# Optimization experiments

Measured on AMD Instinct MI355X. Metric: run time of the kernel, lower is better.

The kernel has to match this reference:

```python
import jax, jax.numpy as jnp
import numpy as np

N, E, B = 50000, 800000, 128
NF, ED, HID, HEADS, DH, OUT, L = 7, 2, 128, 4, 32, 64, 3
EPS = 1e-5
NEG_SLOPE = 0.2


def _layer_norm(x, g, b):
    mu = jnp.mean(x, axis=-1, keepdims=True)
    v = jnp.mean((x - mu) ** 2, axis=-1, keepdims=True)
    return g * (x - mu) / jnp.sqrt(v + EPS) + b


def setup_inputs() -> dict:
    key = jax.random.key(0)
    ks = jax.random.split(key, 32)
    s = 0.05
    inp = {
        "x": jax.random.normal(ks[0], (N, NF), jnp.float32),
        "edge_index": jax.random.randint(ks[1], (2, E), 0, N, jnp.int32),
        "edge_attr": jax.random.uniform(ks[2], (E, ED), jnp.float32),
        "batch": jnp.sort(jax.random.randint(ks[3], (N,), 0, B, jnp.int32)),
        # node encoder
        "enc_W": jax.random.normal(ks[4], (NF, HID)) * (1.0 / np.sqrt(NF)),
        "enc_b": jnp.zeros((HID,)),
        "enc_g": jnp.ones((HID,)),
        "enc_bb": jnp.zeros((HID,)),
        # GATv2 layers (stacked over L)
        "gat_Wsrc": jax.random.normal(ks[5], (L, HID, HID)) * (1.0 / np.sqrt(HID)),
        "gat_Wdst": jax.random.normal(ks[6], (L, HID, HID)) * (1.0 / np.sqrt(HID)),
        "gat_We": jax.random.normal(ks[7], (L, ED, HID)) * (1.0 / np.sqrt(ED)),
        "gat_att": jax.random.normal(ks[8], (L, HEADS, DH)) * s,
        "gat_bias": jnp.zeros((L, HID)),
        # GraphNorm per layer
        "gn_w": jnp.ones((L, HID)),
        "gn_b": jnp.zeros((L, HID)),
        "gn_s": jnp.ones((L, HID)),  # mean_scale
        # attention pooling
        "pool_W1": jax.random.normal(ks[9], (HID, HID)) * (1.0 / np.sqrt(HID)),
        "pool_b1": jnp.zeros((HID,)),
        "pool_W2": jax.random.normal(ks[10], (HID, 1)) * (1.0 / np.sqrt(HID)),
        # output mapper
        "map_W1": jax.random.normal(ks[11], (HID, HID)) * (1.0 / np.sqrt(HID)),
        "map_b1": jnp.zeros((HID,)),
        "map_g": jnp.ones((HID,)),
        "map_bb": jnp.zeros((HID,)),
        "map_W2": jax.random.normal(ks[12], (HID, OUT)) * (1.0 / np.sqrt(HID)),
        "map_b2": jnp.zeros((OUT,)),
    }
    return inp


def _segment_softmax(scores, seg, num_seg):
    # scores: [E2, HEADS], seg: [E2] destination node ids
    m = jax.ops.segment_max(scores, seg, num_segments=num_seg)
    ex = jnp.exp(scores - m[seg])
    denom = jax.ops.segment_sum(ex, seg, num_segments=num_seg)
    return ex / denom[seg]


def _gatv2(x, src, dst, ea, Wsrc, Wdst, We, att, bias):
    e2 = src.shape[0]
    xl = (x @ Wsrc)[src].reshape(e2, HEADS, DH)   # lin_l(x_j), source
    xr = (x @ Wdst)[dst].reshape(e2, HEADS, DH)   # lin_r(x_i), target
    ee = (ea @ We).reshape(e2, HEADS, DH)
    z = jax.nn.leaky_relu(xl + xr + ee, NEG_SLOPE)
    score = jnp.einsum("ehd,hd->eh", z, att)
    alpha = _segment_softmax(score, dst, N)       # softmax over incoming edges
    msg = (xl * alpha[:, :, None]).reshape(e2, HID)
    out = jax.ops.segment_sum(msg, dst, num_segments=N)
    return out + bias


def _graph_norm(x, batch, w, b, scale):
    cnt = jax.ops.segment_sum(jnp.ones((N,), x.dtype), batch, num_segments=B)
    cnt = jnp.maximum(cnt, 1.0)[:, None]
    mean = jax.ops.segment_sum(x, batch, num_segments=B) / cnt
    xc = x - scale * mean[batch]
    var = jax.ops.segment_sum(xc * xc, batch, num_segments=B) / cnt
    return w * xc / jnp.sqrt(var[batch] + EPS) + b


def reference(x, edge_index, edge_attr, batch, enc_W, enc_b, enc_g, enc_bb,
              gat_Wsrc, gat_Wdst, gat_We, gat_att, gat_bias, gn_w, gn_b, gn_s,
              pool_W1, pool_b1, pool_W2, map_W1, map_b1, map_g, map_bb,
              map_W2, map_b2):
    # node encoder: Linear -> ReLU -> LayerNorm
    h = _layer_norm(jax.nn.relu(x @ enc_W + enc_b), enc_g, enc_bb)

    # add self loops; self-loop edge_attr = mean of edge_attr (PyG fill_value='mean')
    loop = jnp.arange(N, dtype=edge_index.dtype)
    src = jnp.concatenate([edge_index[0], loop])
    dst = jnp.concatenate([edge_index[1], loop])
    ea_mean = jnp.mean(edge_attr, axis=0)
    ea = jnp.concatenate([edge_attr, jnp.broadcast_to(ea_mean, (N, ED))], axis=0)

    for i in range(L):
        out = _gatv2(h, src, dst, ea, gat_Wsrc[i], gat_Wdst[i], gat_We[i],
                     gat_att[i], gat_bias[i])
        out = out + h  # residual (in_dim == out_dim -> Identity proj)
        out = _graph_norm(out, batch, gn_w[i], gn_b[i], gn_s[i])
        h = jax.nn.elu(out)

    node_emb = h
    # attention pooling: softmax over ALL nodes (dim=0, as in source)
    scores = jnp.tanh(h @ pool_W1 + pool_b1) @ pool_W2          # [N, 1]
    weights = jax.nn.softmax(scores, axis=0)
    g = jax.ops.segment_sum(h * weights, batch, num_segments=B)  # [B, HID]

    # output mapper (dropout inactive at eval)
    g = _layer_norm(jax.nn.relu(g @ map_W1 + map_b1), map_g, map_bb)
    graph_emb = g @ map_W2 + map_b2
    return graph_emb, node_emb
```

## Files before the change

### kernel.cpp

```cpp
#include <hip/hip_runtime.h>
#include <hip/hip_bf16.h>

typedef __hip_bfloat16 bf16;
typedef __attribute__((ext_vector_type(8))) short short8;
typedef __attribute__((ext_vector_type(4))) float float4v;
typedef float f32x2 __attribute__((ext_vector_type(2)));

#define Nn   50000
#define Ee   800000
#define E2   850000
#define Bb   128
#define NFd  7
#define HID  128
#define OUTD 64
#define EPS  1e-5f
#define SLOPE 0.2f
#define LOG2E 1.4426950408889634f
#define NSTRIP 3125
#define NPAIR  1563

#define MFMA16(a,b,c) __builtin_amdgcn_mfma_f32_16x16x32_bf16(a,b,c,0,0,0)

__device__ __forceinline__ float lane_bcast(float v, int l){
  return __int_as_float(__builtin_amdgcn_readlane(__float_as_int(v), l));
}
__device__ __forceinline__ float wred_sum(float v){
  #pragma unroll
  for (int o=32;o;o>>=1) v += __shfl_xor(v, o, 64);
  return v;
}
#define UPD_DPP(x, ctrl) \
  __int_as_float(__builtin_amdgcn_update_dpp(0, __float_as_int(x), (ctrl), 0xf, 0xf, false))
__device__ __forceinline__ float red4_quad(float x){
  x = x + UPD_DPP(x, 0xB1);
  x = x + UPD_DPP(x, 0x4E);
  return x;
}
__device__ __forceinline__ unsigned fkey(float f){
  unsigned u = __float_as_uint(f);
  return (u & 0x80000000u) ? ~u : (u | 0x80000000u);
}
__device__ __forceinline__ float fkeyinv(unsigned k){
  unsigned u = (k & 0x80000000u) ? (k ^ 0x80000000u) : ~k;
  return __uint_as_float(u);
}
__device__ __forceinline__ float tanh_fast(float x){
  float e = __expf(fminf(fmaxf(2.f*x, -30.f), 30.f));
  return (e-1.f)/(e+1.f);
}
__device__ __forceinline__ float bf_lo(unsigned u){ return __uint_as_float(u<<16); }
__device__ __forceinline__ float bf_hi(unsigned u){ return __uint_as_float(u & 0xffff0000u); }
__device__ __forceinline__ unsigned short f2bs(float f){
  bf16 h = __float2bfloat16(f);
  return *reinterpret_cast<unsigned short*>(&h);
}
__device__ __forceinline__ unsigned pack2(float a, float b){
  return (unsigned)f2bs(a) | ((unsigned)f2bs(b) << 16);
}
__device__ __forceinline__ int xcd_swizzle(int bid, int nwg){
  int q = nwg >> 3, r = nwg & 7;
  int x = bid & 7, i = bid >> 3;
  return (x < r ? x*(q+1) : r*(q+1) + (x-r)*q) + i;
}

__global__ __launch_bounds__(256) void k_wprep(
    const float* __restrict__ gWsrc, const float* __restrict__ gWdst,
    const float* __restrict__ pW1,
    unsigned* __restrict__ wtimg, unsigned* __restrict__ pw1img){
  int idx = blockIdx.x*256 + threadIdx.x;
  if (idx < 3*256*64){
    int l  = idx / (256*64);
    int r  = idx - l*(256*64);
    int n  = r >> 6;
    int kp = r & 63;
    const float* Wp = (n < 128) ? (gWsrc + (size_t)l*HID*HID)
                                : (gWdst + (size_t)l*HID*HID - 128);
    float w0 = Wp[(2*kp)*HID + n];
    float w1 = Wp[(2*kp+1)*HID + n];
    int byt = (n*256 + kp*4) ^ ((n&7)<<4);
    *(unsigned*)((char*)(wtimg + (size_t)l*16384) + byt) = pack2(w0, w1);
  } else {
    int r = idx - 3*256*64;
    if (r < 128*64){
      int n  = r >> 6;
      int kp = r & 63;
      float w0 = pW1[(2*kp)*HID + n];
      float w1 = pW1[(2*kp+1)*HID + n];
      int byt = (n*256 + kp*4) ^ ((n&7)<<4);
      *(unsigned*)((char*)pw1img + byt) = pack2(w0, w1);
    }
  }
}

__global__ __launch_bounds__(256) void k_encoder(
    const float* __restrict__ x, const float* __restrict__ W, const float* __restrict__ b,
    const float* __restrict__ g, const float* __restrict__ bbv,
    unsigned* __restrict__ hbu){
  int wv = (blockIdx.x*blockDim.x + threadIdx.x) >> 6;
  if (wv >= Nn) return;
  int lane = threadIdx.x & 63;
  int d0 = 2*lane, d1 = d0+1;
  float y0 = b[d0], y1 = b[d1];
  #pragma unroll
  for (int i=0;i<NFd;++i){
    float xv = x[wv*NFd + i];
    y0 = fmaf(xv, W[i*HID + d0], y0);
    y1 = fmaf(xv, W[i*HID + d1], y1);
  }
  y0 = fmaxf(y0, 0.f); y1 = fmaxf(y1, 0.f);
  float mu = wred_sum(y0+y1) * (1.f/HID);
  float c0 = y0-mu, c1 = y1-mu;
  float var = wred_sum(c0*c0 + c1*c1) * (1.f/HID);
  float rs = rsqrtf(var + EPS);
  float v0 = g[d0]*c0*rs + bbv[d0];
  float v1 = g[d1]*c1*rs + bbv[d1];
  hbu[(size_t)wv*64 + lane] = pack2(v0, v1);
}

__global__ void k_ea_mean(const float* __restrict__ ea, float* __restrict__ eam){
  int tid = blockIdx.x*blockDim.x + threadIdx.x;
  const float2* ea2 = (const float2*)ea;
  float a0=0.f, a1=0.f;
  for (int e=tid; e<Ee; e += gridDim.x*blockDim.x){
    float2 v = ea2[e];
    a0 += v.x; a1 += v.y;
  }
  a0 = wred_sum(a0); a1 = wred_sum(a1);
  if ((threadIdx.x & 63)==0){
    atomicAdd(&eam[0], a0*(1.f/Ee));
    atomicAdd(&eam[1], a1*(1.f/Ee));
  }
}

__global__ void k_deg(const int* __restrict__ ei, int* __restrict__ deg){
  int e = blockIdx.x*blockDim.x + threadIdx.x;
  if (e >= E2) return;
  int d = (e < Ee) ? ei[Ee + e] : (e - Ee);
  atomicAdd(&deg[d], 1);
}

__global__ __launch_bounds__(1024) void k_scan(const int* __restrict__ deg,
    int* __restrict__ offs, int* __restrict__ cursor){
  __shared__ int wsum[16];
  __shared__ int tot_s;
  __shared__ int carry_s;
  int t = threadIdx.x, lane = t & 63, wid = t >> 6;
  if (t==0) carry_s = 0;
  __syncthreads();
  for (int base=0; base<Nn; base += 4096){
    int i0 = base + t*4;
    int v0=0,v1=0,v2=0,v3=0;
    if (i0+3 < Nn){
      int4 qv = *(const int4*)(deg + i0);
      v0=qv.x; v1=qv.y; v2=qv.z; v3=qv.w;
    } else {
      if (i0   < Nn) v0 = deg[i0];
      if (i0+1 < Nn) v1 = deg[i0+1];
      if (i0+2 < Nn) v2 = deg[i0+2];
      if (i0+3 < Nn) v3 = deg[i0+3];
    }
    int tot = v0+v1+v2+v3;
    int x = tot;
    #pragma unroll
    for (int o=1;o<64;o<<=1){ int u = __shfl_up(x, o, 64); if (lane >= o) x += u; }
    if (lane==63) wsum[wid] = x;
    __syncthreads();
    if (t==0){ int s=0; for (int k=0;k<16;++k){ int tv=wsum[k]; wsum[k]=s; s+=tv; } tot_s = s; }
    __syncthreads();
    int excl = carry_s + wsum[wid] + (x - tot);
    int p0 = excl, p1 = excl+v0, p2 = p1+v1, p3 = p2+v2;
    if (i0+3 < Nn){
      *(int4*)(offs + i0)   = make_int4(p0,p1,p2,p3);
      *(int4*)(cursor + i0) = make_int4(p0,p1,p2,p3);
    } else {
      if (i0   < Nn){ offs[i0]  =p0; cursor[i0]  =p0; }
      if (i0+1 < Nn){ offs[i0+1]=p1; cursor[i0+1]=p1; }
      if (i0+2 < Nn){ offs[i0+2]=p2; cursor[i0+2]=p2; }
      if (i0+3 < Nn){ offs[i0+3]=p3; cursor[i0+3]=p3; }
    }
    __syncthreads();
    if (t==0) carry_s += tot_s;
    __syncthreads();
  }
  if (t==0) offs[Nn] = carry_s;
}

__global__ void k_scatter(const int* __restrict__ ei, const float* __restrict__ ea,
    const float* __restrict__ eam, int* __restrict__ cursor,
    int* __restrict__ csrc, float2* __restrict__ cea){
  int e = blockIdx.x*blockDim.x + threadIdx.x;
  if (e >= E2 + 8) return;
  if (e >= E2){
    csrc[e] = 0;
    cea[e] = make_float2(0.f, 0.f);
    return;
  }
  int s, d; float a0, a1;
  if (e < Ee){
    s = ei[e]; d = ei[Ee + e];
    float2 v = ((const float2*)ea)[e];
    a0 = v.x; a1 = v.y;
  } else {
    s = d = e - Ee; a0 = eam[0]; a1 = eam[1];
  }
  int pos = atomicAdd(&cursor[d], 1);
  csrc[pos] = s;
  cea[pos] = make_float2(a0, a1);
}

__global__ void k_gstart(const int* __restrict__ batch, int* __restrict__ gstart){
  int n = blockIdx.x*blockDim.x + threadIdx.x;
  if (n >= Nn) return;
  int bc = batch[n];
  int bp = (n==0) ? -1 : batch[n-1];
  for (int b = bp+1; b <= bc; ++b) gstart[b] = n;
  if (n == Nn-1){ for (int b = bc+1; b <= Bb; ++b) gstart[b] = Nn; }
}

__global__ __launch_bounds__(256) void k_dualgemm(
    const unsigned* __restrict__ hbu, const unsigned* __restrict__ wtimg,
    unsigned* __restrict__ hsb, float* __restrict__ hd){
  __shared__ unsigned wt[16384];
  for (int i = threadIdx.x; i < 4096; i += 256)
    ((uint4*)wt)[i] = ((const uint4*)wtimg)[i];
  __syncthreads();
  int wid = threadIdx.x >> 6, lane = threadIdx.x & 63;
  int q = lane >> 4, c = lane & 15;
  const unsigned short* hb = (const unsigned short*)hbu;
  for (int pr = blockIdx.x*4 + wid; pr < NPAIR; pr += gridDim.x*4){
    int p0 = 2*pr, p1 = 2*pr + 1;
    bool v1 = (p1 < NSTRIP);
    int node0 = p0*16 + c;
    int node1 = v1 ? (p1*16 + c) : node0;
    short8 bf0[4], bf1[4];
    const unsigned short* hp0 = hb + (size_t)node0*HID + q*8;
    const unsigned short* hp1 = hb + (size_t)node1*HID + q*8;
    #pragma unroll
    for (int s=0;s<4;++s){
      bf0[s] = *(const short8*)(hp0 + s*32);
      bf1[s] = *(const short8*)(hp1 + s*32);
    }
    #pragma unroll 4
    for (int t=0;t<16;++t){
      float4v ac0 = {0.f,0.f,0.f,0.f}, ac1 = {0.f,0.f,0.f,0.f};
      #pragma unroll
      for (int s=0;s<4;++s){
        int row = t*16 + c;
        int byt = (row*256 + s*64 + q*16) ^ ((row&7)<<4);
        short8 af = *(const short8*)((const char*)wt + byt);
        ac0 = MFMA16(af, bf0[s], ac0);
        ac1 = MFMA16(af, bf1[s], ac1);
      }
      if (t < 8){
        int co = t*8 + q*2;
        *(uint2*)(hsb + (size_t)node0*64 + co) =
            make_uint2(pack2(ac0[0],ac0[1]), pack2(ac0[2],ac0[3]));
        if (v1) *(uint2*)(hsb + (size_t)node1*64 + co) =
            make_uint2(pack2(ac1[0],ac1[1]), pack2(ac1[2],ac1[3]));
      } else {
        int dd = (t-8)*16 + q*4;
        *(float4*)(hd + (size_t)node0*HID + dd) = make_float4(ac0[0],ac0[1],ac0[2],ac0[3]);
        if (v1) *(float4*)(hd + (size_t)node1*HID + dd) = make_float4(ac1[0],ac1[1],ac1[2],ac1[3]);
      }
    }
  }
}

__global__ __launch_bounds__(256) void k_edge(const unsigned* __restrict__ hsb,
    float* __restrict__ hdio, const unsigned* __restrict__ hbu,
    const int* __restrict__ csrc, const float2* __restrict__ cea,
    const int* __restrict__ offs, const float* __restrict__ We,
    const float* __restrict__ att, const float* __restrict__ bias){
  int bid = xcd_swizzle(blockIdx.x, gridDim.x);
  int n = (bid*256 + (int)threadIdx.x) >> 6;
  if (n >= Nn) return;
  int lane = threadIdx.x & 63;
  int row = lane >> 4;
  int c   = lane & 15;
  int d0  = 8*c;
  f32x2 we0v[4], we1v[4], atv[4], xrv[4];
  #pragma unroll
  for (int k=0;k<4;++k){
    we0v[k] = *(const f32x2*)(We + d0 + 2*k);
    we1v[k] = *(const f32x2*)(We + HID + d0 + 2*k);
    f32x2 a = *(const f32x2*)(att + d0 + 2*k);
    atv[k]  = a * LOG2E;
    xrv[k]  = *(const f32x2*)(hdio + (size_t)n*HID + d0 + 2*k);
  }
  int e0 = offs[n], e1 = offs[n+1];
  float m = 0.f, ssum = 0.f;
  f32x2 accv[4];
  #pragma unroll
  for (int k=0;k<4;++k) accv[k] = (f32x2){0.f,0.f};

  int   sC = csrc[e0 + row];
  float2 eC = cea[e0 + row];
  uint4 xC = *(const uint4*)(hsb + ((size_t)(unsigned)sC<<6) + 4*c);
  bool  vC = (e0 + row) < e1;
  for (int e = e0; e < e1; e += 4){
    int en = e + 4 + row;
    int   sN = csrc[en];
    float2 eN = cea[en];
    uint4 xN = *(const uint4*)(hsb + ((size_t)(unsigned)sN<<6) + 4*c);
    bool  vN = en < e1;
    f32x2 xl2[4];
    xl2[0] = (f32x2){bf_lo(xC.x), bf_hi(xC.x)};
    xl2[1] = (f32x2){bf_lo(xC.y), bf_hi(xC.y)};
    xl2[2] = (f32x2){bf_lo(xC.z), bf_hi(xC.z)};
    xl2[3] = (f32x2){bf_lo(xC.w), bf_hi(xC.w)};
    f32x2 ex2 = (f32x2){eC.x, eC.x};
    f32x2 ey2 = (f32x2){eC.y, eC.y};
    f32x2 dotv = (f32x2){0.f, 0.f};
    #pragma unroll
    for (int k=0;k<4;++k){
      f32x2 z = __builtin_elementwise_fma(ey2, we1v[k],
                  __builtin_elementwise_fma(ex2, we0v[k], xl2[k] + xrv[k]));
      z = __builtin_elementwise_max(z, z * SLOPE);
      dotv = __builtin_elementwise_fma(z, atv[k], dotv);
    }
    float sc = red4_quad(dotv.x + dotv.y);
    if (e == e0) m = __shfl(sc, lane & 15, 64);
    float p = exp2f(sc - m);
    p = vC ? p : 0.f;
    ssum += p;
    f32x2 pv = (f32x2){p, p};
    #pragma unroll
    for (int k=0;k<4;++k) accv[k] = __builtin_elementwise_fma(pv, xl2[k], accv[k]);
    sC=sN; eC=eN; xC=xN; vC=vN;
  }
  float acc[8];
  #pragma unroll
  for (int k=0;k<4;++k){ acc[2*k] = accv[k].x; acc[2*k+1] = accv[k].y; }
  #pragma unroll
  for (int j=0;j<8;++j){
    acc[j] += __shfl_xor(acc[j], 16, 64);
    acc[j] += __shfl_xor(acc[j], 32, 64);
  }
  ssum += __shfl_xor(ssum, 16, 64);
  ssum += __shfl_xor(ssum, 32, 64);
  if (row == 0){
    float inv = 1.f/ssum;
    uint4 hu = *(const uint4*)(hbu + ((size_t)n<<6) + 4*c);
    float hr[8];
    hr[0]=bf_lo(hu.x); hr[1]=bf_hi(hu.x); hr[2]=bf_lo(hu.y); hr[3]=bf_hi(hu.y);
    hr[4]=bf_lo(hu.z); hr[5]=bf_hi(hu.z); hr[6]=bf_lo(hu.w); hr[7]=bf_hi(hu.w);
    float o[8];
    #pragma unroll
    for (int j=0;j<8;++j) o[j] = fmaf(acc[j], inv, bias[d0+j] + hr[j]);
    *(float4*)(hdio + (size_t)n*HID + d0)     = make_float4(o[0],o[1],o[2],o[3]);
    *(float4*)(hdio + (size_t)n*HID + d0 + 4) = make_float4(o[4],o[5],o[6],o[7]);
  }
}

__global__ __launch_bounds__(128) void k_gn_reduce(const float* __restrict__ out,
    const int* __restrict__ gstart, float* __restrict__ gsum_, float* __restrict__ gsq_){
  int b = blockIdx.x >> 4, sub = blockIdx.x & 15;
  int ns = gstart[b], ne = gstart[b+1];
  int d = threadIdx.x;
  float s = 0.f, qq = 0.f;
  for (int n = ns + sub; n < ne; n += 16){
    float v = out[(size_t)n*HID + d];
    s += v; qq = fmaf(v, v, qq);
  }
  atomicAdd(&gsum_[b*HID + d], s);
  atomicAdd(&gsq_[b*HID + d], qq);
}

__global__ __launch_bounds__(256) void k_gn_apply(const float* __restrict__ out,
    const float* __restrict__ gsum_, const float* __restrict__ gsq_,
    const int* __restrict__ gstart, const int* __restrict__ batch,
    const float* __restrict__ gw, const float* __restrict__ gb,
    const float* __restrict__ gs,
    unsigned* __restrict__ hbu, float* __restrict__ emb){
  int n = (blockIdx.x*blockDim.x + threadIdx.x) >> 6;
  if (n >= Nn) return;
  int lane = threadIdx.x & 63;
  int b = batch[n];
  float icnt = 1.f / fmaxf((float)(gstart[b+1]-gstart[b]), 1.f);
  int d0 = 2*lane, d1 = d0+1;
  float2 x = *(const float2*)(out + (size_t)n*HID + d0);
  float mean0 = gsum_[b*HID+d0]*icnt, mean1 = gsum_[b*HID+d1]*icnt;
  float ms0 = mean0*gs[d0], ms1 = mean1*gs[d1];
  float var0 = gsq_[b*HID+d0]*icnt - ms0*(2.f*mean0 - ms0);
  float var1 = gsq_[b*HID+d1]*icnt - ms1*(2.f*mean1 - ms1);
  float rs0 = rsqrtf(fmaxf(var0, 0.f) + EPS);
  float rs1 = rsqrtf(fmaxf(var1, 0.f) + EPS);
  float y0 = gw[d0]*(x.x - ms0)*rs0 + gb[d0];
  float y1 = gw[d1]*(x.y - ms1)*rs1 + gb[d1];
  y0 = (y0 > 0.f) ? y0 : (__expf(y0) - 1.f);
  y1 = (y1 > 0.f) ? y1 : (__expf(y1) - 1.f);
  hbu[(size_t)n*64 + lane] = pack2(y0, y1);
  if (emb) *(float2*)(emb + (size_t)n*HID + d0) = make_float2(y0, y1);
}

__global__ __launch_bounds__(256) void k_pool_score(
    const unsigned* __restrict__ hbu, const unsigned* __restrict__ pw1img,
    const float* __restrict__ b1, const float* __restrict__ W2,
    float* __restrict__ score, unsigned* __restrict__ mkey){
  __shared__ unsigned wt[8192];
  __shared__ float b1l[HID], w2l[HID];
  for (int i = threadIdx.x; i < 2048; i += 256)
    ((uint4*)wt)[i] = ((const uint4*)pw1img)[i];
  if (threadIdx.x < HID){ b1l[threadIdx.x] = b1[threadIdx.x]; w2l[threadIdx.x] = W2[threadIdx.x]; }
  __syncthreads();
  int wid = threadIdx.x >> 6, lane = threadIdx.x & 63;
  int q = lane >> 4, c = lane & 15;
  const unsigned short* hb = (const unsigned short*)hbu;
  float bmax = -1e30f;
  for (int p = blockIdx.x*4 + wid; p < NSTRIP; p += gridDim.x*4){
    int node = p*16 + c;
    short8 bf[4];
    const unsigned short* hp = hb + (size_t)node*HID + q*8;
    #pragma unroll
    for (int s=0;s<4;++s) bf[s] = *(const short8*)(hp + s*32);
    float part = 0.f;
    #pragma unroll
    for (int t=0;t<8;++t){
      float4v ac = {0.f,0.f,0.f,0.f};
      #pragma unroll
      for (int s=0;s<4;++s){
        int row = t*16 + c;
        int byt = (row*256 + s*64 + q*16) ^ ((row&7)<<4);
        ac = MFMA16(*(const short8*)((const char*)wt + byt), bf[s], ac);
      }
      int dim = t*16 + q*4;
      #pragma unroll
      for (int r=0;r<4;++r)
        part += tanh_fast(ac[r] + b1l[dim+r]) * w2l[dim+r];
    }
    part += __shfl_xor(part, 16, 64);
    part += __shfl_xor(part, 32, 64);
    if (q==0) score[node] = part;
    bmax = fmaxf(bmax, part);
  }
  #pragma unroll
  for (int o=32;o;o>>=1) bmax = fmaxf(bmax, __shfl_xor(bmax, o, 64));
  if (lane==0) atomicMax(mkey, fkey(bmax));
}

__global__ __launch_bounds__(128) void k_pool_reduce(const unsigned* __restrict__ hbu,
    const float* __restrict__ score, const unsigned* __restrict__ mkey,
    const int* __restrict__ gstart, float* __restrict__ gsum, float* __restrict__ total){
  int b = blockIdx.x >> 4, sub = blockIdx.x & 15;
  int ns = gstart[b], ne = gstart[b+1];
  float mx = fkeyinv(*mkey);
  int d = threadIdx.x;
  float acc = 0.f, es = 0.f;
  for (int n = ns + sub; n < ne; n += 16){
    float ev = __expf(score[n] - mx);
    unsigned u = hbu[(size_t)n*64 + (d>>1)];
    float hv = (d & 1) ? bf_hi(u) : bf_lo(u);
    acc = fmaf(ev, hv, acc);
    if (d==0) es += ev;
  }
  atomicAdd(&gsum[b*HID + d], acc);
  if (d==0) atomicAdd(total, es);
}

__global__ __launch_bounds__(64) void k_mapper(const float* __restrict__ gsum,
    const float* __restrict__ total,
    const float* __restrict__ W1, const float* __restrict__ b1,
    const float* __restrict__ g,  const float* __restrict__ bbv,
    const float* __restrict__ W2, const float* __restrict__ b2v,
    float* __restrict__ out0){
  int b = blockIdx.x, lane = threadIdx.x;
  float inv = 1.f/(*total);
  int d0 = 2*lane, d1 = d0+1;
  float gv0 = gsum[b*HID + d0]*inv, gv1 = gsum[b*HID + d1]*inv;
  float a0 = b1[d0], a1 = b1[d1];
  for (int i=0;i<HID;++i){
    float hv = lane_bcast((i&1) ? gv1 : gv0, i>>1);
    a0 = fmaf(hv, W1[i*HID + d0], a0);
    a1 = fmaf(hv, W1[i*HID + d1], a1);
  }
  a0 = fmaxf(a0, 0.f); a1 = fmaxf(a1, 0.f);
  float mu = wred_sum(a0+a1) * (1.f/HID);
  float c0 = a0-mu, c1 = a1-mu;
  float var = wred_sum(c0*c0 + c1*c1) * (1.f/HID);
  float rs = rsqrtf(var + EPS);
  float l0 = g[d0]*c0*rs + bbv[d0];
  float l1 = g[d1]*c1*rs + bbv[d1];
  float acc = b2v[lane];
  for (int j=0;j<HID;++j){
    float lv = lane_bcast((j&1) ? l1 : l0, j>>1);
    acc = fmaf(lv, W2[j*OUTD + lane], acc);
  }
  out0[b*OUTD + lane] = acc;
}

extern "C" void kernel_launch(void* const* d_in, const int* in_sizes, int n_in,
                              void* d_out, int out_size, void* d_ws, size_t ws_size,
                              hipStream_t stream){
  const float* x     = (const float*)d_in[0];
  const int*   ei    = (const int*)  d_in[1];
  const float* ea    = (const float*)d_in[2];
  const int*   batch = (const int*)  d_in[3];
  const float* encW  = (const float*)d_in[4];
  const float* encb  = (const float*)d_in[5];
  const float* encg  = (const float*)d_in[6];
  const float* encbb = (const float*)d_in[7];
  const float* gWsrc = (const float*)d_in[8];
  const float* gWdst = (const float*)d_in[9];
  const float* gWe   = (const float*)d_in[10];
  const float* gatt  = (const float*)d_in[11];
  const float* gbias = (const float*)d_in[12];
  const float* gnw   = (const float*)d_in[13];
  const float* gnb   = (const float*)d_in[14];
  const float* gns   = (const float*)d_in[15];
  const float* pW1   = (const float*)d_in[16];
  const float* pb1   = (const float*)d_in[17];
  const float* pW2   = (const float*)d_in[18];
  const float* mW1   = (const float*)d_in[19];
  const float* mb1   = (const float*)d_in[20];
  const float* mg    = (const float*)d_in[21];
  const float* mbb   = (const float*)d_in[22];
  const float* mW2   = (const float*)d_in[23];
  const float* mb2   = (const float*)d_in[24];

  char* w = (char*)d_ws;
  size_t off = 0;
  auto alloc = [&](size_t bytes)->char*{
    char* p = w + off;
    off += (bytes + 255) & ~(size_t)255;
    return p;
  };
  unsigned* hbu    = (unsigned*)alloc((size_t)Nn*64*4);
  unsigned* hsb    = (unsigned*)alloc((size_t)Nn*64*4);
  float*    hd     = (float*)   alloc((size_t)Nn*HID*4);
  int*      csrc   = (int*)     alloc((size_t)(E2+8)*4);
  float2*   cea    = (float2*)  alloc((size_t)(E2+8)*8);
  int*      offs   = (int*)     alloc((size_t)(Nn+1)*4);
  int*      cursor = (int*)     alloc((size_t)Nn*4);
  int*      deg    = (int*)     alloc((size_t)Nn*4);
  int*      gstart = (int*)     alloc((size_t)(Bb+1)*4);
  float*    score  = (float*)   alloc((size_t)Nn*4);
  float*    gsum   = (float*)   alloc((size_t)Bb*HID*4 * 7);
  float*    gnbase = gsum + Bb*HID;
  unsigned* wtimg  = (unsigned*)alloc((size_t)3*16384*4);
  unsigned* pw1img = (unsigned*)alloc((size_t)8192*4);
  float*    scal   = (float*)   alloc(256);
  float*    eam   = scal;
  float*    total = scal + 2;
  unsigned* mkey  = (unsigned*)(scal + 3);

  float* out_graph = (float*)d_out;
  float* out_node  = (float*)d_out + (size_t)Bb*OUTD;

  hipMemsetAsync(deg,  0, (size_t)Nn*4, stream);
  hipMemsetAsync(scal, 0, 256, stream);
  hipMemsetAsync(gsum, 0, (size_t)Bb*HID*4 * 7, stream);

  k_wprep<<<224, 256, 0, stream>>>(gWsrc, gWdst, pW1, wtimg, pw1img);
  k_encoder<<<Nn/4, 256, 0, stream>>>(x, encW, encb, encg, encbb, hbu);
  k_ea_mean<<<256, 256, 0, stream>>>(ea, eam);
  k_deg<<<(E2+255)/256, 256, 0, stream>>>(ei, deg);
  k_scan<<<1, 1024, 0, stream>>>(deg, offs, cursor);
  k_scatter<<<(E2+8+255)/256, 256, 0, stream>>>(ei, ea, eam, cursor, csrc, cea);
  k_gstart<<<(Nn+255)/256, 256, 0, stream>>>(batch, gstart);

  for (int l = 0; l < 3; ++l){
    float* gnsum_l = gnbase + (size_t)l*2*Bb*HID;
    float* gnsq_l  = gnsum_l + Bb*HID;
    k_dualgemm<<<392, 256, 0, stream>>>(hbu, wtimg + (size_t)l*16384, hsb, hd);
    k_edge<<<Nn/4, 256, 0, stream>>>(hsb, hd, hbu, csrc, cea, offs,
                                     gWe + (size_t)l*2*HID,
                                     gatt + (size_t)l*4*32,
                                     gbias + (size_t)l*HID);
    k_gn_reduce<<<Bb*16, 128, 0, stream>>>(hd, gstart, gnsum_l, gnsq_l);
    k_gn_apply<<<Nn/4, 256, 0, stream>>>(hd, gnsum_l, gnsq_l, gstart, batch,
                                         gnw + (size_t)l*HID, gnb + (size_t)l*HID,
                                         gns + (size_t)l*HID, hbu,
                                         (l==2) ? out_node : (float*)nullptr);
  }

  k_pool_score<<<256, 256, 0, stream>>>(hbu, pw1img, pb1, pW2, score, mkey);
  k_pool_reduce<<<Bb*16, 128, 0, stream>>>(hbu, score, mkey, gstart, gsum, total);
  k_mapper<<<Bb, 64, 0, stream>>>(gsum, total, mW1, mb1, mg, mbb, mW2, mb2, out_graph);
}
```

Baseline: 551.1 us.

## Pack edge src/attr into int4, deepen edge prefetch, fuse degree count

```diff
diff --git a/kernel.cpp b/kernel.cpp
--- a/kernel.cpp
+++ b/kernel.cpp
@@ -117,26 +117,21 @@
   hbu[(size_t)wv*64 + lane] = pack2(v0, v1);
 }
 
-__global__ void k_ea_mean(const float* __restrict__ ea, float* __restrict__ eam){
+__global__ void k_ea_deg(const int* __restrict__ ei, const float* __restrict__ ea,
+    int* __restrict__ deg, float* __restrict__ eam){
   int tid = blockIdx.x*blockDim.x + threadIdx.x;
   const float2* ea2 = (const float2*)ea;
   float a0=0.f, a1=0.f;
   for (int e=tid; e<Ee; e += gridDim.x*blockDim.x){
     float2 v = ea2[e];
     a0 += v.x; a1 += v.y;
+    atomicAdd(&deg[ei[Ee + e]], 1);
   }
   a0 = wred_sum(a0); a1 = wred_sum(a1);
   if ((threadIdx.x & 63)==0){
     atomicAdd(&eam[0], a0*(1.f/Ee));
     atomicAdd(&eam[1], a1*(1.f/Ee));
   }
-}
-
-__global__ void k_deg(const int* __restrict__ ei, int* __restrict__ deg){
-  int e = blockIdx.x*blockDim.x + threadIdx.x;
-  if (e >= E2) return;
-  int d = (e < Ee) ? ei[Ee + e] : (e - Ee);
-  atomicAdd(&deg[d], 1);
 }
 
 __global__ __launch_bounds__(1024) void k_scan(const int* __restrict__ deg,
@@ -152,12 +147,12 @@
     int v0=0,v1=0,v2=0,v3=0;
     if (i0+3 < Nn){
       int4 qv = *(const int4*)(deg + i0);
-      v0=qv.x; v1=qv.y; v2=qv.z; v3=qv.w;
+      v0=qv.x+1; v1=qv.y+1; v2=qv.z+1; v3=qv.w+1;
     } else {
-      if (i0   < Nn) v0 = deg[i0];
-      if (i0+1 < Nn) v1 = deg[i0+1];
-      if (i0+2 < Nn) v2 = deg[i0+2];
-      if (i0+3 < Nn) v3 = deg[i0+3];
+      if (i0   < Nn) v0 = deg[i0]+1;
+      if (i0+1 < Nn) v1 = deg[i0+1]+1;
+      if (i0+2 < Nn) v2 = deg[i0+2]+1;
+      if (i0+3 < Nn) v3 = deg[i0+3]+1;
     }
     int tot = v0+v1+v2+v3;
     int x = tot;
@@ -187,12 +182,11 @@
 
 __global__ void k_scatter(const int* __restrict__ ei, const float* __restrict__ ea,
     const float* __restrict__ eam, int* __restrict__ cursor,
-    int* __restrict__ csrc, float2* __restrict__ cea){
+    int4* __restrict__ ecomb){
   int e = blockIdx.x*blockDim.x + threadIdx.x;
-  if (e >= E2 + 8) return;
+  if (e >= E2 + 16) return;
   if (e >= E2){
-    csrc[e] = 0;
-    cea[e] = make_float2(0.f, 0.f);
+    ecomb[e] = make_int4(0, 0, 0, 0);
     return;
   }
   int s, d; float a0, a1;
@@ -204,8 +198,7 @@
     s = d = e - Ee; a0 = eam[0]; a1 = eam[1];
   }
   int pos = atomicAdd(&cursor[d], 1);
-  csrc[pos] = s;
-  cea[pos] = make_float2(a0, a1);
+  ecomb[pos] = make_int4(s, __float_as_int(a0), __float_as_int(a1), 0);
 }
 
 __global__ void k_gstart(const int* __restrict__ batch, int* __restrict__ gstart){
@@ -268,7 +261,7 @@
 
 __global__ __launch_bounds__(256) void k_edge(const unsigned* __restrict__ hsb,
     float* __restrict__ hdio, const unsigned* __restrict__ hbu,
-    const int* __restrict__ csrc, const float2* __restrict__ cea,
+    const int4* __restrict__ ecomb,
     const int* __restrict__ offs, const float* __restrict__ We,
     const float* __restrict__ att, const float* __restrict__ bias){
   int bid = xcd_swizzle(blockIdx.x, gridDim.x);
@@ -293,23 +286,22 @@
   #pragma unroll
   for (int k=0;k<4;++k) accv[k] = (f32x2){0.f,0.f};
 
-  int   sC = csrc[e0 + row];
-  float2 eC = cea[e0 + row];
-  uint4 xC = *(const uint4*)(hsb + ((size_t)(unsigned)sC<<6) + 4*c);
-  bool  vC = (e0 + row) < e1;
+  int4  r0 = ecomb[e0 + row];
+  uint4 x0 = *(const uint4*)(hsb + ((size_t)(unsigned)r0.x<<6) + 4*c);
+  int4  r1 = ecomb[e0 + 4 + row];
+  uint4 x1 = *(const uint4*)(hsb + ((size_t)(unsigned)r1.x<<6) + 4*c);
   for (int e = e0; e < e1; e += 4){
-    int en = e + 4 + row;
-    int   sN = csrc[en];
-    float2 eN = cea[en];
-    uint4 xN = *(const uint4*)(hsb + ((size_t)(unsigned)sN<<6) + 4*c);
-    bool  vN = en < e1;
+    int4  r2 = ecomb[e + 8 + row];
+    uint4 x2 = *(const uint4*)(hsb + ((size_t)(unsigned)r2.x<<6) + 4*c);
+    bool vC = (e + row) < e1;
     f32x2 xl2[4];
-    xl2[0] = (f32x2){bf_lo(xC.x), bf_hi(xC.x)};
-    xl2[1] = (f32x2){bf_lo(xC.y), bf_hi(xC.y)};
-    xl2[2] = (f32x2){bf_lo(xC.z), bf_hi(xC.z)};
-    xl2[3] = (f32x2){bf_lo(xC.w), bf_hi(xC.w)};
-    f32x2 ex2 = (f32x2){eC.x, eC.x};
-    f32x2 ey2 = (f32x2){eC.y, eC.y};
+    xl2[0] = (f32x2){bf_lo(x0.x), bf_hi(x0.x)};
+    xl2[1] = (f32x2){bf_lo(x0.y), bf_hi(x0.y)};
+    xl2[2] = (f32x2){bf_lo(x0.z), bf_hi(x0.z)};
+    xl2[3] = (f32x2){bf_lo(x0.w), bf_hi(x0.w)};
+    float ex = __int_as_float(r0.y), ey = __int_as_float(r0.z);
+    f32x2 ex2 = (f32x2){ex, ex};
+    f32x2 ey2 = (f32x2){ey, ey};
     f32x2 dotv = (f32x2){0.f, 0.f};
     #pragma unroll
     for (int k=0;k<4;++k){
@@ -326,7 +318,7 @@
     f32x2 pv = (f32x2){p, p};
     #pragma unroll
     for (int k=0;k<4;++k) accv[k] = __builtin_elementwise_fma(pv, xl2[k], accv[k]);
-    sC=sN; eC=eN; xC=xN; vC=vN;
+    r0=r1; x0=x1; r1=r2; x1=x2;
   }
   float acc[8];
   #pragma unroll
@@ -527,8 +519,7 @@
   unsigned* hbu    = (unsigned*)alloc((size_t)Nn*64*4);
   unsigned* hsb    = (unsigned*)alloc((size_t)Nn*64*4);
   float*    hd     = (float*)   alloc((size_t)Nn*HID*4);
-  int*      csrc   = (int*)     alloc((size_t)(E2+8)*4);
-  float2*   cea    = (float2*)  alloc((size_t)(E2+8)*8);
+  int4*     ecomb  = (int4*)    alloc((size_t)(E2+16)*16);
   int*      offs   = (int*)     alloc((size_t)(Nn+1)*4);
   int*      cursor = (int*)     alloc((size_t)Nn*4);
   int*      deg    = (int*)     alloc((size_t)Nn*4);
@@ -552,17 +543,16 @@
 
   k_wprep<<<224, 256, 0, stream>>>(gWsrc, gWdst, pW1, wtimg, pw1img);
   k_encoder<<<Nn/4, 256, 0, stream>>>(x, encW, encb, encg, encbb, hbu);
-  k_ea_mean<<<256, 256, 0, stream>>>(ea, eam);
-  k_deg<<<(E2+255)/256, 256, 0, stream>>>(ei, deg);
+  k_ea_deg<<<1024, 256, 0, stream>>>(ei, ea, deg, eam);
   k_scan<<<1, 1024, 0, stream>>>(deg, offs, cursor);
-  k_scatter<<<(E2+8+255)/256, 256, 0, stream>>>(ei, ea, eam, cursor, csrc, cea);
+  k_scatter<<<(E2+16+255)/256, 256, 0, stream>>>(ei, ea, eam, cursor, ecomb);
   k_gstart<<<(Nn+255)/256, 256, 0, stream>>>(batch, gstart);
 
   for (int l = 0; l < 3; ++l){
     float* gnsum_l = gnbase + (size_t)l*2*Bb*HID;
     float* gnsq_l  = gnsum_l + Bb*HID;
     k_dualgemm<<<392, 256, 0, stream>>>(hbu, wtimg + (size_t)l*16384, hsb, hd);
-    k_edge<<<Nn/4, 256, 0, stream>>>(hsb, hd, hbu, csrc, cea, offs,
+    k_edge<<<Nn/4, 256, 0, stream>>>(hsb, hd, hbu, ecomb, offs,
                                      gWe + (size_t)l*2*HID,
                                      gatt + (size_t)l*4*32,
                                      gbias + (size_t)l*HID);
```

Measured after the change: 610.8 us. +10.8%, slower.
